# Kernel optimization log

Hardware: AMD Instinct MI355X
Metric: run time of the kernel (lower is better)

## Reference

```python
import jax, jax.numpy as jnp
import numpy as np

B, S, D, H = 4, 2048, 1024, 16
DK = D // H  # d_k = d_v = 64


def setup_inputs() -> dict:
    key = jax.random.key(0)
    ks = jax.random.split(key, 9)
    sc = 0.02
    return {
        "x": jax.random.normal(ks[0], (B, S, D), dtype=jnp.float32),
        "Wq": jax.random.normal(ks[1], (H, D, DK), dtype=jnp.float32) * sc,
        "bq": jax.random.normal(ks[2], (H, DK), dtype=jnp.float32) * sc,
        "Wk": jax.random.normal(ks[3], (H, D, DK), dtype=jnp.float32) * sc,
        "bk": jax.random.normal(ks[4], (H, DK), dtype=jnp.float32) * sc,
        "Wv": jax.random.normal(ks[5], (H, D, DK), dtype=jnp.float32) * sc,
        "bv": jax.random.normal(ks[6], (H, DK), dtype=jnp.float32) * sc,
        "Wo": jax.random.normal(ks[7], (D, D), dtype=jnp.float32) * sc,
        "bo": jax.random.normal(ks[8], (D,), dtype=jnp.float32) * sc,
    }


def reference(x, Wq, bq, Wk, bk, Wv, bv, Wo, bo):
    # per-head learned projections (heads stacked on leading axis h)
    Q = jnp.einsum("bsd,hdk->bhsk", x, Wq) + bq[None, :, None, :]
    K = jnp.einsum("bsd,hdk->bhsk", x, Wk) + bk[None, :, None, :]
    V = jnp.einsum("bsd,hdk->bhsk", x, Wv) + bv[None, :, None, :]
    scores = jnp.einsum("bhsk,bhtk->bhst", Q, K) / jnp.sqrt(jnp.float32(DK))
    # causal mask: future_sight=0, past_sight=None -> positions t > s replaced by -1e9
    s_idx = jnp.arange(S)
    causal = s_idx[:, None] >= s_idx[None, :]  # [S, S] True where allowed
    scores = jnp.where(causal[None, None, :, :], scores, jnp.float32(-1e9))
    attn = jax.nn.softmax(scores, axis=-1)
    out = jnp.einsum("bhst,bhtk->bhsk", attn, V)  # [B, H, S, DK]
    # concat heads along feature dim (head order matches ModuleList order)
    cat = out.transpose(0, 2, 1, 3).reshape(B, S, D)
    return cat @ Wo + bo
```

## Files before the change

### kernel.cpp

```cpp
#include <hip/hip_runtime.h>
#include <stdint.h>

#define B_  4
#define S_  2048
#define D_  1024
#define H_  16
#define DK_ 64
#define M_  (B_ * S_)

typedef __attribute__((ext_vector_type(8))) short bf16x8;
typedef __attribute__((ext_vector_type(4))) float f32x4;

__device__ __forceinline__ uint16_t f2bf(float f) {
    uint32_t u = __builtin_bit_cast(uint32_t, f);
    u = (u + 0x7FFFu + ((u >> 16) & 1u)) >> 16;
    return (uint16_t)u;
}

__global__ __launch_bounds__(256) void cvt_bf16_kernel(const float* __restrict__ in,
                                                       uint16_t* __restrict__ out, int n) {
    int i = (blockIdx.x * 256 + threadIdx.x) * 8;
    if (i >= n) return;
    float4 a = *(const float4*)&in[i];
    float4 b = *(const float4*)&in[i + 4];
    uint16_t o[8] = {f2bf(a.x), f2bf(a.y), f2bf(a.z), f2bf(a.w),
                     f2bf(b.x), f2bf(b.y), f2bf(b.z), f2bf(b.w)};
    *(uint4*)&out[i] = *(const uint4*)o;
}

__global__ __launch_bounds__(256) void transpose_cvt_kernel(
    const float* __restrict__ in, uint16_t* __restrict__ out, int R, int C) {
    __shared__ __align__(16) uint16_t tile[64][72];
    const int mat = blockIdx.z;
    const float* inm = in + (size_t)mat * R * C;
    uint16_t* outm = out + (size_t)mat * R * C;
    const int r0 = blockIdx.x * 64, c0 = blockIdx.y * 64;
    const int t = threadIdx.x;
    const int lr = t >> 2, lc = (t & 3) * 16;
    uint16_t tmp[16];
    #pragma unroll
    for (int j = 0; j < 16; j += 4) {
        float4 v = *(const float4*)&inm[(size_t)(r0 + lr) * C + c0 + lc + j];
        tmp[j] = f2bf(v.x); tmp[j + 1] = f2bf(v.y); tmp[j + 2] = f2bf(v.z); tmp[j + 3] = f2bf(v.w);
    }
    *(uint4*)&tile[lr][lc]     = ((const uint4*)tmp)[0];
    *(uint4*)&tile[lr][lc + 8] = ((const uint4*)tmp)[1];
    __syncthreads();
    const int oc = t >> 2, orr = (t & 3) * 16;
    uint16_t ot[16];
    #pragma unroll
    for (int j = 0; j < 16; ++j) ot[j] = tile[orr + j][oc];
    *(uint4*)&outm[(size_t)(c0 + oc) * R + r0 + orr]     = ((const uint4*)ot)[0];
    *(uint4*)&outm[(size_t)(c0 + oc) * R + r0 + orr + 8] = ((const uint4*)ot)[1];
}

__global__ __launch_bounds__(256) void qkv_mfma_kernel(
    const uint16_t* __restrict__ xb, const uint16_t* __restrict__ Wt,
    const float* __restrict__ bq, const float* __restrict__ bk, const float* __restrict__ bv,
    uint16_t* __restrict__ Q, uint16_t* __restrict__ K, uint16_t* __restrict__ V)
{
    __shared__ __align__(16) uint16_t As[128][72];
    __shared__ __align__(16) uint16_t Bs[128][72];
    const int tid = threadIdx.x;
    const int nb = blockIdx.x;
    const int sel = nb >> 3, npair = nb & 7;
    const int m0 = blockIdx.y * 128;
    const int lane = tid & 63, w = tid >> 6;
    const int wr = w >> 1, wc = w & 1;
    const int ll = lane & 15, quad = lane >> 4;

    const uint16_t* Bg = Wt + (size_t)nb * 128 * 1024;
    const float* bias = (sel == 0) ? bq : (sel == 1) ? bk : bv;
    uint16_t* Out = (sel == 0) ? Q : (sel == 1) ? K : V;

    const int ar = tid >> 1, ac = (tid & 1) * 32;

    f32x4 acc[4][4];
    const f32x4 zz = {0.f, 0.f, 0.f, 0.f};
    #pragma unroll
    for (int i = 0; i < 4; ++i)
        #pragma unroll
        for (int j = 0; j < 4; ++j) acc[i][j] = zz;

    for (int k0 = 0; k0 < 1024; k0 += 64) {
        __syncthreads();
        const uint16_t* ag = &xb[(size_t)(m0 + ar) * 1024 + k0 + ac];
        uint4 a0 = *(const uint4*)(ag);
        uint4 a1 = *(const uint4*)(ag + 8);
        uint4 a2 = *(const uint4*)(ag + 16);
        uint4 a3 = *(const uint4*)(ag + 24);
        const uint16_t* bg = &Bg[(size_t)ar * 1024 + k0 + ac];
        uint4 b0 = *(const uint4*)(bg);
        uint4 b1 = *(const uint4*)(bg + 8);
        uint4 b2 = *(const uint4*)(bg + 16);
        uint4 b3 = *(const uint4*)(bg + 24);
        *(uint4*)&As[ar][ac]      = a0;
        *(uint4*)&As[ar][ac + 8]  = a1;
        *(uint4*)&As[ar][ac + 16] = a2;
        *(uint4*)&As[ar][ac + 24] = a3;
        *(uint4*)&Bs[ar][ac]      = b0;
        *(uint4*)&Bs[ar][ac + 8]  = b1;
        *(uint4*)&Bs[ar][ac + 16] = b2;
        *(uint4*)&Bs[ar][ac + 24] = b3;
        __syncthreads();
        #pragma unroll
        for (int ks = 0; ks < 2; ++ks) {
            bf16x8 af[4], bfv[4];
            #pragma unroll
            for (int mt = 0; mt < 4; ++mt)
                af[mt] = *(const bf16x8*)&As[wr * 64 + mt * 16 + ll][ks * 32 + quad * 8];
            #pragma unroll
            for (int nt = 0; nt < 4; ++nt)
                bfv[nt] = *(const bf16x8*)&Bs[wc * 64 + nt * 16 + ll][ks * 32 + quad * 8];
            #pragma unroll
            for (int mt = 0; mt < 4; ++mt)
                #pragma unroll
                for (int nt = 0; nt < 4; ++nt)
                    acc[mt][nt] = __builtin_amdgcn_mfma_f32_16x16x32_bf16(af[mt], bfv[nt], acc[mt][nt], 0, 0, 0);
        }
    }

    const float qscale = (sel == 0) ? 0.125f : 1.0f;
    #pragma unroll
    for (int nt = 0; nt < 4; ++nt) {
        const int nl = wc * 64 + nt * 16 + ll;
        const int hh = npair * 2 + (nl >> 6);
        const int dk = nl & 63;
        const float bval = bias[npair * 128 + nl];
        #pragma unroll
        for (int mt = 0; mt < 4; ++mt) {
            #pragma unroll
            for (int r = 0; r < 4; ++r) {
                int m = m0 + wr * 64 + mt * 16 + quad * 4 + r;
                int b = m >> 11, s = m & 2047;
                float v = (acc[mt][nt][r] + bval) * qscale;
                Out[((size_t)(b * 16 + hh) * 2048 + s) * 64 + dk] = f2bf(v);
            }
        }
    }
}

__global__ __launch_bounds__(256) void attn_mfma_kernel(
    const uint16_t* __restrict__ Q, const uint16_t* __restrict__ K,
    const uint16_t* __restrict__ V, uint16_t* __restrict__ CAT)
{
    __shared__ __align__(16) uint16_t Qs[128][72];
    __shared__ __align__(16) uint16_t Ks[64][72];
    __shared__ __align__(16) uint16_t Vt[64][72];
    __shared__ __align__(16) uint16_t Ps[128][72];
    __shared__ __align__(16) float rbuf[128];

    const int tid = threadIdx.x;
    const int lane = tid & 63, w = tid >> 6;
    const int ll = lane & 15, quad = lane >> 4;
    const int bh = blockIdx.y;
    const int b = bh >> 4, h = bh & 15;

    const uint16_t* Qbh = Q + (size_t)bh * S_ * 64;
    const uint16_t* Kbh = K + (size_t)bh * S_ * 64;
    const uint16_t* Vbh = V + (size_t)bh * S_ * 64;
    uint16_t* Cbh = CAT + (size_t)b * 2048 * 1024 + h * 64;

    #pragma unroll 1
    for (int phase = 0; phase < 2; ++phase) {
        const int qtb = phase == 0 ? (15 - (int)blockIdx.x) : (int)blockIdx.x;
        const int q0 = qtb * 128;

        {
            const int r = tid >> 1, c = (tid & 1) * 32;
            const uint16_t* g = &Qbh[(size_t)(q0 + r) * 64 + c];
            uint4 v0 = *(const uint4*)g, v1 = *(const uint4*)(g + 8);
            uint4 v2 = *(const uint4*)(g + 16), v3 = *(const uint4*)(g + 24);
            *(uint4*)&Qs[r][c] = v0;      *(uint4*)&Qs[r][c + 8] = v1;
            *(uint4*)&Qs[r][c + 16] = v2; *(uint4*)&Qs[r][c + 24] = v3;
        }
        __syncthreads();

        bf16x8 qf[2][2];
        #pragma unroll
        for (int nt = 0; nt < 2; ++nt)
            #pragma unroll
            for (int ks = 0; ks < 2; ++ks)
                qf[nt][ks] = *(const bf16x8*)&Qs[w * 32 + nt * 16 + ll][ks * 32 + quad * 8];

        float l_run[2] = {0.f, 0.f};
        f32x4 oacc[2][4];
        const f32x4 zz = {0.f, 0.f, 0.f, 0.f};
        #pragma unroll
        for (int i = 0; i < 2; ++i)
            #pragma unroll
            for (int j = 0; j < 4; ++j) oacc[i][j] = zz;

        const int qw = q0 + w * 32;
        const int ktmax = 2 * qtb + 1;

        for (int kt = 0; kt <= ktmax; ++kt) {
            const int tb = kt * 64;
            __syncthreads();
            {
                const int r = tid >> 2, c = (tid & 3) * 16;
                const uint16_t* g = &Kbh[(size_t)(tb + r) * 64 + c];
                uint4 v0 = *(const uint4*)g, v1 = *(const uint4*)(g + 8);
                *(uint4*)&Ks[r][c] = v0;
                *(uint4*)&Ks[r][c + 8] = v1;
            }
            {
                const int tp = (tid & 31) * 2, d0 = (tid >> 5) * 8;
                const uint16_t* g0 = &Vbh[(size_t)(tb + tp) * 64 + d0];
                uint16_t lo[8], hi[8];
                *(uint4*)lo = *(const uint4*)g0;
                *(uint4*)hi = *(const uint4*)(g0 + 64);
                #pragma unroll
                for (int j = 0; j < 8; ++j) {
                    uint32_t pk = (uint32_t)lo[j] | ((uint32_t)hi[j] << 16);
                    *(uint32_t*)&Vt[d0 + j][tp] = pk;
                }
            }
            __syncthreads();

            const bool active = (tb <= qw + 31);
            if (active) {
                f32x4 sacc[4][2];
                #pragma unroll
                for (int i = 0; i < 4; ++i)
                    #pragma unroll
                    for (int j = 0; j < 2; ++j) sacc[i][j] = zz;
                #pragma unroll
                for (int ks = 0; ks < 2; ++ks) {
                    bf16x8 kf[4];
                    #pragma unroll
                    for (int tt = 0; tt < 4; ++tt)
                        kf[tt] = *(const bf16x8*)&Ks[tt * 16 + ll][ks * 32 + quad * 8];
                    #pragma unroll
                    for (int tt = 0; tt < 4; ++tt)
                        #pragma unroll
                        for (int nt = 0; nt < 2; ++nt)
                            sacc[tt][nt] = __builtin_amdgcn_mfma_f32_16x16x32_bf16(kf[tt], qf[nt][ks], sacc[tt][nt], 0, 0, 0);
                }
                const bool needMask = (tb + 63 > qw);
                #pragma unroll
                for (int nt = 0; nt < 2; ++nt) {
                    const int qg = qw + nt * 16 + ll;
                    float ls = 0.f;
                    #pragma unroll
                    for (int tt = 0; tt < 4; ++tt) {
                        #pragma unroll
                        for (int r = 0; r < 4; ++r) {
                            float v = sacc[tt][nt][r];
                            if (needMask) {
                                int tg = tb + tt * 16 + quad * 4 + r;
                                v = (tg > qg) ? -1e30f : v;
                            }
                            float p = __expf(v);
                            sacc[tt][nt][r] = p;
                            ls += p;
                        }
                    }
                    ls += __shfl_xor(ls, 16);
                    ls += __shfl_xor(ls, 32);
                    l_run[nt] += ls;
                    #pragma unroll
                    for (int tt = 0; tt < 4; ++tt) {
                        uint2 pv;
                        pv.x = (uint32_t)f2bf(sacc[tt][nt][0]) | ((uint32_t)f2bf(sacc[tt][nt][1]) << 16);
                        pv.y = (uint32_t)f2bf(sacc[tt][nt][2]) | ((uint32_t)f2bf(sacc[tt][nt][3]) << 16);
                        *(uint2*)&Ps[w * 32 + nt * 16 + ll][tt * 16 + quad * 4] = pv;
                    }
                }
            }
            __syncthreads();
            if (active) {
                #pragma unroll
                for (int ks = 0; ks < 2; ++ks) {
                    bf16x8 pf[2], vf[4];
                    #pragma unroll
                    for (int mt = 0; mt < 2; ++mt)
                        pf[mt] = *(const bf16x8*)&Ps[w * 32 + mt * 16 + ll][ks * 32 + quad * 8];
                    #pragma unroll
                    for (int nt = 0; nt < 4; ++nt)
                        vf[nt] = *(const bf16x8*)&Vt[nt * 16 + ll][ks * 32 + quad * 8];
                    #pragma unroll
                    for (int mt = 0; mt < 2; ++mt)
                        #pragma unroll
                        for (int nt = 0; nt < 4; ++nt)
                            oacc[mt][nt] = __builtin_amdgcn_mfma_f32_16x16x32_bf16(pf[mt], vf[nt], oacc[mt][nt], 0, 0, 0);
                }
            }
        }

        if (quad == 0) {
            rbuf[w * 32 + ll]      = 1.f / l_run[0];
            rbuf[w * 32 + 16 + ll] = 1.f / l_run[1];
        }
        __syncthreads();
        #pragma unroll
        for (int mt = 0; mt < 2; ++mt) {
            f32x4 li = *(const f32x4*)&rbuf[w * 32 + mt * 16 + quad * 4];
            #pragma unroll
            for (int r = 0; r < 4; ++r) {
                int q = q0 + w * 32 + mt * 16 + quad * 4 + r;
                #pragma unroll
                for (int nt = 0; nt < 4; ++nt) {
                    float v = oacc[mt][nt][r] * li[r];
                    Cbh[(size_t)q * 1024 + nt * 16 + ll] = f2bf(v);
                }
            }
        }
        __syncthreads();
    }
}

__global__ __launch_bounds__(256) void oproj_mfma_kernel(
    const uint16_t* __restrict__ CATb, const uint16_t* __restrict__ Wot,
    const float* __restrict__ bo, float* __restrict__ out)
{
    __shared__ __align__(16) uint16_t As[128][72];
    __shared__ __align__(16) uint16_t Bs[128][72];
    const int tid = threadIdx.x;
    const int n0 = blockIdx.x * 128;
    const int m0 = blockIdx.y * 128;
    const int lane = tid & 63, w = tid >> 6;
    const int wr = w >> 1, wc = w & 1;
    const int ll = lane & 15, quad = lane >> 4;

    const int ar = tid >> 1, ac = (tid & 1) * 32;

    f32x4 acc[4][4];
    const f32x4 zz = {0.f, 0.f, 0.f, 0.f};
    #pragma unroll
    for (int i = 0; i < 4; ++i)
        #pragma unroll
        for (int j = 0; j < 4; ++j) acc[i][j] = zz;

    for (int k0 = 0; k0 < 1024; k0 += 64) {
        __syncthreads();
        const uint16_t* ag = &CATb[(size_t)(m0 + ar) * 1024 + k0 + ac];
        uint4 a0 = *(const uint4*)(ag);
        uint4 a1 = *(const uint4*)(ag + 8);
        uint4 a2 = *(const uint4*)(ag + 16);
        uint4 a3 = *(const uint4*)(ag + 24);
        const uint16_t* bg = &Wot[(size_t)(n0 + ar) * 1024 + k0 + ac];
        uint4 b0 = *(const uint4*)(bg);
        uint4 b1 = *(const uint4*)(bg + 8);
        uint4 b2 = *(const uint4*)(bg + 16);
        uint4 b3 = *(const uint4*)(bg + 24);
        *(uint4*)&As[ar][ac]      = a0;
        *(uint4*)&As[ar][ac + 8]  = a1;
        *(uint4*)&As[ar][ac + 16] = a2;
        *(uint4*)&As[ar][ac + 24] = a3;
        *(uint4*)&Bs[ar][ac]      = b0;
        *(uint4*)&Bs[ar][ac + 8]  = b1;
        *(uint4*)&Bs[ar][ac + 16] = b2;
        *(uint4*)&Bs[ar][ac + 24] = b3;
        __syncthreads();
        #pragma unroll
        for (int ks = 0; ks < 2; ++ks) {
            bf16x8 af[4], bfv[4];
            #pragma unroll
            for (int mt = 0; mt < 4; ++mt)
                af[mt] = *(const bf16x8*)&As[wr * 64 + mt * 16 + ll][ks * 32 + quad * 8];
            #pragma unroll
            for (int nt = 0; nt < 4; ++nt)
                bfv[nt] = *(const bf16x8*)&Bs[wc * 64 + nt * 16 + ll][ks * 32 + quad * 8];
            #pragma unroll
            for (int mt = 0; mt < 4; ++mt)
                #pragma unroll
                for (int nt = 0; nt < 4; ++nt)
                    acc[mt][nt] = __builtin_amdgcn_mfma_f32_16x16x32_bf16(af[mt], bfv[nt], acc[mt][nt], 0, 0, 0);
        }
    }

    #pragma unroll
    for (int nt = 0; nt < 4; ++nt) {
        const int nl = wc * 64 + nt * 16 + ll;
        const float bval = bo[n0 + nl];
        #pragma unroll
        for (int mt = 0; mt < 4; ++mt) {
            #pragma unroll
            for (int r = 0; r < 4; ++r) {
                int m = m0 + wr * 64 + mt * 16 + quad * 4 + r;
                out[(size_t)m * 1024 + n0 + nl] = acc[mt][nt][r] + bval;
            }
        }
    }
}

extern "C" void kernel_launch(void* const* d_in, const int* in_sizes, int n_in,
                              void* d_out, int out_size, void* d_ws, size_t ws_size,
                              hipStream_t stream) {
    const float* x  = (const float*)d_in[0];
    const float* Wq = (const float*)d_in[1];
    const float* bq = (const float*)d_in[2];
    const float* Wk = (const float*)d_in[3];
    const float* bk = (const float*)d_in[4];
    const float* Wv = (const float*)d_in[5];
    const float* bv = (const float*)d_in[6];
    const float* Wo = (const float*)d_in[7];
    const float* bo = (const float*)d_in[8];

    uint8_t* p = (uint8_t*)d_ws;
    uint16_t* xb   = (uint16_t*)p; p += (size_t)M_ * D_ * 2;
    uint16_t* Wt   = (uint16_t*)p; p += (size_t)3 * H_ * DK_ * D_ * 2;
    uint16_t* Wot  = (uint16_t*)p; p += (size_t)D_ * D_ * 2;
    uint16_t* Qb   = (uint16_t*)p; p += (size_t)B_ * H_ * S_ * DK_ * 2;
    uint16_t* Kb   = (uint16_t*)p; p += (size_t)B_ * H_ * S_ * DK_ * 2;
    uint16_t* Vb   = (uint16_t*)p; p += (size_t)B_ * H_ * S_ * DK_ * 2;
    uint16_t* CATb = (uint16_t*)p;

    cvt_bf16_kernel<<<dim3((M_ * D_) / 2048), 256, 0, stream>>>(x, xb, M_ * D_);
    transpose_cvt_kernel<<<dim3(D_ / 64, 1, H_), 256, 0, stream>>>(Wq, Wt, D_, DK_);
    transpose_cvt_kernel<<<dim3(D_ / 64, 1, H_), 256, 0, stream>>>(Wk, Wt + (size_t)H_ * DK_ * D_, D_, DK_);
    transpose_cvt_kernel<<<dim3(D_ / 64, 1, H_), 256, 0, stream>>>(Wv, Wt + (size_t)2 * H_ * DK_ * D_, D_, DK_);
    transpose_cvt_kernel<<<dim3(D_ / 64, D_ / 64, 1), 256, 0, stream>>>(Wo, Wot, D_, D_);

    qkv_mfma_kernel<<<dim3(24, M_ / 128), 256, 0, stream>>>(xb, Wt, bq, bk, bv, Qb, Kb, Vb);
    attn_mfma_kernel<<<dim3(8, B_ * H_), 256, 0, stream>>>(Qb, Kb, Vb, CATb);
    oproj_mfma_kernel<<<dim3(8, M_ / 128), 256, 0, stream>>>(CATb, Wot, bo, (float*)d_out);
}
```

Before: 290.7 us.

## Store V transposed from QKV, shrink attention query tile, use exp2 softmax

The QKV projection now writes V transposed (head, dk, seq) with packed bf16 stores, so the attention kernel loads V tiles directly into LDS without the per-element transpose shuffle. The attention kernel drops to 64-query tiles per phase with Q fragments read straight from global memory, and the grid doubles to 16 blocks per head. Q is pre-scaled by log2(e)/8 so the softmax uses exp2f, and a perm-based packer replaces the scalar bf16 conversions. The new packer rounds half-up instead of to nearest-even, and the smaller tiles mean more K/V tile reloads per query in exchange for more parallelism.

```diff
diff --git a/kernel.cpp b/kernel.cpp
--- a/kernel.cpp
+++ b/kernel.cpp
@@ -11,10 +11,18 @@
 typedef __attribute__((ext_vector_type(8))) short bf16x8;
 typedef __attribute__((ext_vector_type(4))) float f32x4;
 
+#define QSCALE 0.1803368801111204f
+
 __device__ __forceinline__ uint16_t f2bf(float f) {
     uint32_t u = __builtin_bit_cast(uint32_t, f);
     u = (u + 0x7FFFu + ((u >> 16) & 1u)) >> 16;
     return (uint16_t)u;
+}
+
+__device__ __forceinline__ uint32_t pk2bf(float hi, float lo) {
+    uint32_t a = __builtin_bit_cast(uint32_t, hi) + 0x8000u;
+    uint32_t b = __builtin_bit_cast(uint32_t, lo) + 0x8000u;
+    return __builtin_amdgcn_perm(a, b, 0x07060302u);
 }
 
 __global__ __launch_bounds__(256) void cvt_bf16_kernel(const float* __restrict__ in,
@@ -71,7 +79,6 @@
 
     const uint16_t* Bg = Wt + (size_t)nb * 128 * 1024;
     const float* bias = (sel == 0) ? bq : (sel == 1) ? bk : bv;
-    uint16_t* Out = (sel == 0) ? Q : (sel == 1) ? K : V;
 
     const int ar = tid >> 1, ac = (tid & 1) * 32;
 
@@ -120,21 +127,41 @@
         }
     }
 
-    const float qscale = (sel == 0) ? 0.125f : 1.0f;
-    #pragma unroll
-    for (int nt = 0; nt < 4; ++nt) {
-        const int nl = wc * 64 + nt * 16 + ll;
-        const int hh = npair * 2 + (nl >> 6);
-        const int dk = nl & 63;
-        const float bval = bias[npair * 128 + nl];
-        #pragma unroll
-        for (int mt = 0; mt < 4; ++mt) {
-            #pragma unroll
-            for (int r = 0; r < 4; ++r) {
-                int m = m0 + wr * 64 + mt * 16 + quad * 4 + r;
+    if (sel == 2) {
+        #pragma unroll
+        for (int nt = 0; nt < 4; ++nt) {
+            const int nl = wc * 64 + nt * 16 + ll;
+            const int hh = npair * 2 + (nl >> 6);
+            const int dk = nl & 63;
+            const float bval = bias[npair * 128 + nl];
+            #pragma unroll
+            for (int mt = 0; mt < 4; ++mt) {
+                int m = m0 + wr * 64 + mt * 16 + quad * 4;
                 int b = m >> 11, s = m & 2047;
-                float v = (acc[mt][nt][r] + bval) * qscale;
-                Out[((size_t)(b * 16 + hh) * 2048 + s) * 64 + dk] = f2bf(v);
+                uint2 pv;
+                pv.x = pk2bf(acc[mt][nt][1] + bval, acc[mt][nt][0] + bval);
+                pv.y = pk2bf(acc[mt][nt][3] + bval, acc[mt][nt][2] + bval);
+                *(uint2*)&V[((size_t)(b * 16 + hh) * 64 + dk) * 2048 + s] = pv;
+            }
+        }
+    } else {
+        uint16_t* Out = (sel == 0) ? Q : K;
+        const float qs = (sel == 0) ? QSCALE : 1.0f;
+        #pragma unroll
+        for (int nt = 0; nt < 4; ++nt) {
+            const int nl = wc * 64 + nt * 16 + ll;
+            const int hh = npair * 2 + (nl >> 6);
+            const int dk = nl & 63;
+            const float bval = bias[npair * 128 + nl];
+            #pragma unroll
+            for (int mt = 0; mt < 4; ++mt) {
+                #pragma unroll
+                for (int r = 0; r < 4; ++r) {
+                    int m = m0 + wr * 64 + mt * 16 + quad * 4 + r;
+                    int b = m >> 11, s = m & 2047;
+                    float v = (acc[mt][nt][r] + bval) * qs;
+                    Out[((size_t)(b * 16 + hh) * 2048 + s) * 64 + dk] = f2bf(v);
+                }
             }
         }
     }
@@ -142,168 +169,123 @@
 
 __global__ __launch_bounds__(256) void attn_mfma_kernel(
     const uint16_t* __restrict__ Q, const uint16_t* __restrict__ K,
-    const uint16_t* __restrict__ V, uint16_t* __restrict__ CAT)
+    const uint16_t* __restrict__ Vg, uint16_t* __restrict__ CAT)
 {
-    __shared__ __align__(16) uint16_t Qs[128][72];
     __shared__ __align__(16) uint16_t Ks[64][72];
     __shared__ __align__(16) uint16_t Vt[64][72];
-    __shared__ __align__(16) uint16_t Ps[128][72];
-    __shared__ __align__(16) float rbuf[128];
+    __shared__ __align__(16) uint16_t Ps[64][72];
+    __shared__ __align__(16) float rbuf[64];
 
     const int tid = threadIdx.x;
     const int lane = tid & 63, w = tid >> 6;
     const int ll = lane & 15, quad = lane >> 4;
+    const int p = blockIdx.x;
     const int bh = blockIdx.y;
     const int b = bh >> 4, h = bh & 15;
 
     const uint16_t* Qbh = Q + (size_t)bh * S_ * 64;
     const uint16_t* Kbh = K + (size_t)bh * S_ * 64;
-    const uint16_t* Vbh = V + (size_t)bh * S_ * 64;
+    const uint16_t* Vbh = Vg + (size_t)bh * 64 * S_;
     uint16_t* Cbh = CAT + (size_t)b * 2048 * 1024 + h * 64;
+
+    const int sr = tid >> 2, sc = (tid & 3) * 16;
 
     #pragma unroll 1
     for (int phase = 0; phase < 2; ++phase) {
-        const int qtb = phase == 0 ? (15 - (int)blockIdx.x) : (int)blockIdx.x;
-        const int q0 = qtb * 128;
-
-        {
-            const int r = tid >> 1, c = (tid & 1) * 32;
-            const uint16_t* g = &Qbh[(size_t)(q0 + r) * 64 + c];
-            uint4 v0 = *(const uint4*)g, v1 = *(const uint4*)(g + 8);
-            uint4 v2 = *(const uint4*)(g + 16), v3 = *(const uint4*)(g + 24);
-            *(uint4*)&Qs[r][c] = v0;      *(uint4*)&Qs[r][c + 8] = v1;
-            *(uint4*)&Qs[r][c + 16] = v2; *(uint4*)&Qs[r][c + 24] = v3;
-        }
-        __syncthreads();
-
-        bf16x8 qf[2][2];
-        #pragma unroll
-        for (int nt = 0; nt < 2; ++nt)
-            #pragma unroll
-            for (int ks = 0; ks < 2; ++ks)
-                qf[nt][ks] = *(const bf16x8*)&Qs[w * 32 + nt * 16 + ll][ks * 32 + quad * 8];
-
-        float l_run[2] = {0.f, 0.f};
-        f32x4 oacc[2][4];
+        const int qtb = (phase == 0) ? (31 - p) : p;
+        const int q0 = qtb * 64;
+        const int qw = q0 + w * 16;
+        const int qg = qw + ll;
+
+        bf16x8 qf[2];
+        #pragma unroll
+        for (int ks = 0; ks < 2; ++ks)
+            qf[ks] = *(const bf16x8*)&Qbh[(size_t)(qw + ll) * 64 + ks * 32 + quad * 8];
+
+        float l_run = 0.f;
+        f32x4 oacc[4];
         const f32x4 zz = {0.f, 0.f, 0.f, 0.f};
         #pragma unroll
-        for (int i = 0; i < 2; ++i)
-            #pragma unroll
-            for (int j = 0; j < 4; ++j) oacc[i][j] = zz;
-
-        const int qw = q0 + w * 32;
-        const int ktmax = 2 * qtb + 1;
-
-        for (int kt = 0; kt <= ktmax; ++kt) {
+        for (int j = 0; j < 4; ++j) oacc[j] = zz;
+
+        for (int kt = 0; kt <= qtb; ++kt) {
             const int tb = kt * 64;
             __syncthreads();
             {
-                const int r = tid >> 2, c = (tid & 3) * 16;
-                const uint16_t* g = &Kbh[(size_t)(tb + r) * 64 + c];
+                const uint16_t* g = &Kbh[(size_t)(tb + sr) * 64 + sc];
                 uint4 v0 = *(const uint4*)g, v1 = *(const uint4*)(g + 8);
-                *(uint4*)&Ks[r][c] = v0;
-                *(uint4*)&Ks[r][c + 8] = v1;
+                *(uint4*)&Ks[sr][sc] = v0;
+                *(uint4*)&Ks[sr][sc + 8] = v1;
             }
             {
-                const int tp = (tid & 31) * 2, d0 = (tid >> 5) * 8;
-                const uint16_t* g0 = &Vbh[(size_t)(tb + tp) * 64 + d0];
-                uint16_t lo[8], hi[8];
-                *(uint4*)lo = *(const uint4*)g0;
-                *(uint4*)hi = *(const uint4*)(g0 + 64);
-                #pragma unroll
-                for (int j = 0; j < 8; ++j) {
-                    uint32_t pk = (uint32_t)lo[j] | ((uint32_t)hi[j] << 16);
-                    *(uint32_t*)&Vt[d0 + j][tp] = pk;
+                const uint16_t* g = &Vbh[(size_t)sr * 2048 + tb + sc];
+                uint4 v0 = *(const uint4*)g, v1 = *(const uint4*)(g + 8);
+                *(uint4*)&Vt[sr][sc] = v0;
+                *(uint4*)&Vt[sr][sc + 8] = v1;
+            }
+            __syncthreads();
+
+            f32x4 sacc[4];
+            #pragma unroll
+            for (int i = 0; i < 4; ++i) sacc[i] = zz;
+            #pragma unroll
+            for (int ks = 0; ks < 2; ++ks) {
+                #pragma unroll
+                for (int tt = 0; tt < 4; ++tt) {
+                    bf16x8 kf = *(const bf16x8*)&Ks[tt * 16 + ll][ks * 32 + quad * 8];
+                    sacc[tt] = __builtin_amdgcn_mfma_f32_16x16x32_bf16(kf, qf[ks], sacc[tt], 0, 0, 0);
                 }
             }
+
+            const bool needMask = (tb + 63 > qw);
+            float ls = 0.f;
+            #pragma unroll
+            for (int tt = 0; tt < 4; ++tt) {
+                #pragma unroll
+                for (int r = 0; r < 4; ++r) {
+                    float v = sacc[tt][r];
+                    if (needMask) {
+                        int tg = tb + tt * 16 + quad * 4 + r;
+                        v = (tg > qg) ? -1e30f : v;
+                    }
+                    float pe = exp2f(v);
+                    sacc[tt][r] = pe;
+                    ls += pe;
+                }
+            }
+            ls += __shfl_xor(ls, 16);
+            ls += __shfl_xor(ls, 32);
+            l_run += ls;
+            #pragma unroll
+            for (int tt = 0; tt < 4; ++tt) {
+                uint2 pv;
+                pv.x = pk2bf(sacc[tt][1], sacc[tt][0]);
+                pv.y = pk2bf(sacc[tt][3], sacc[tt][2]);
+                *(uint2*)&Ps[w * 16 + ll][tt * 16 + quad * 4] = pv;
+            }
             __syncthreads();
 
-            const bool active = (tb <= qw + 31);
-            if (active) {
-                f32x4 sacc[4][2];
-                #pragma unroll
-                for (int i = 0; i < 4; ++i)
-                    #pragma unroll
-                    for (int j = 0; j < 2; ++j) sacc[i][j] = zz;
-                #pragma unroll
-                for (int ks = 0; ks < 2; ++ks) {
-                    bf16x8 kf[4];
-                    #pragma unroll
-                    for (int tt = 0; tt < 4; ++tt)
-                        kf[tt] = *(const bf16x8*)&Ks[tt * 16 + ll][ks * 32 + quad * 8];
-                    #pragma unroll
-                    for (int tt = 0; tt < 4; ++tt)
-                        #pragma unroll
-                        for (int nt = 0; nt < 2; ++nt)
-                            sacc[tt][nt] = __builtin_amdgcn_mfma_f32_16x16x32_bf16(kf[tt], qf[nt][ks], sacc[tt][nt], 0, 0, 0);
+            #pragma unroll
+            for (int ks = 0; ks < 2; ++ks) {
+                bf16x8 pf = *(const bf16x8*)&Ps[w * 16 + ll][ks * 32 + quad * 8];
+                #pragma unroll
+                for (int nt = 0; nt < 4; ++nt) {
+                    bf16x8 vf = *(const bf16x8*)&Vt[nt * 16 + ll][ks * 32 + quad * 8];
+                    oacc[nt] = __builtin_amdgcn_mfma_f32_16x16x32_bf16(pf, vf, oacc[nt], 0, 0, 0);
                 }
-                const bool needMask = (tb + 63 > qw);
-                #pragma unroll
-                for (int nt = 0; nt < 2; ++nt) {
-                    const int qg = qw + nt * 16 + ll;
-                    float ls = 0.f;
-                    #pragma unroll
-                    for (int tt = 0; tt < 4; ++tt) {
-                        #pragma unroll
-                        for (int r = 0; r < 4; ++r) {
-                            float v = sacc[tt][nt][r];
-                            if (needMask) {
-                                int tg = tb + tt * 16 + quad * 4 + r;
-                                v = (tg > qg) ? -1e30f : v;
-                            }
-                            float p = __expf(v);
-                            sacc[tt][nt][r] = p;
-                            ls += p;
-                        }
-                    }
-                    ls += __shfl_xor(ls, 16);
-                    ls += __shfl_xor(ls, 32);
-                    l_run[nt] += ls;
-                    #pragma unroll
-                    for (int tt = 0; tt < 4; ++tt) {
-                        uint2 pv;
-                        pv.x = (uint32_t)f2bf(sacc[tt][nt][0]) | ((uint32_t)f2bf(sacc[tt][nt][1]) << 16);
-                        pv.y = (uint32_t)f2bf(sacc[tt][nt][2]) | ((uint32_t)f2bf(sacc[tt][nt][3]) << 16);
-                        *(uint2*)&Ps[w * 32 + nt * 16 + ll][tt * 16 + quad * 4] = pv;
-                    }
-                }
-            }
-            __syncthreads();
-            if (active) {
-                #pragma unroll
-                for (int ks = 0; ks < 2; ++ks) {
-                    bf16x8 pf[2], vf[4];
-                    #pragma unroll
-                    for (int mt = 0; mt < 2; ++mt)
-                        pf[mt] = *(const bf16x8*)&Ps[w * 32 + mt * 16 + ll][ks * 32 + quad * 8];
-                    #pragma unroll
-                    for (int nt = 0; nt < 4; ++nt)
-                        vf[nt] = *(const bf16x8*)&Vt[nt * 16 + ll][ks * 32 + quad * 8];
-                    #pragma unroll
-                    for (int mt = 0; mt < 2; ++mt)
-                        #pragma unroll
-                        for (int nt = 0; nt < 4; ++nt)
-                            oacc[mt][nt] = __builtin_amdgcn_mfma_f32_16x16x32_bf16(pf[mt], vf[nt], oacc[mt][nt], 0, 0, 0);
-                }
-            }
-        }
-
-        if (quad == 0) {
-            rbuf[w * 32 + ll]      = 1.f / l_run[0];
-            rbuf[w * 32 + 16 + ll] = 1.f / l_run[1];
-        }
-        __syncthreads();
-        #pragma unroll
-        for (int mt = 0; mt < 2; ++mt) {
-            f32x4 li = *(const f32x4*)&rbuf[w * 32 + mt * 16 + quad * 4];
-            #pragma unroll
-            for (int r = 0; r < 4; ++r) {
-                int q = q0 + w * 32 + mt * 16 + quad * 4 + r;
-                #pragma unroll
-                for (int nt = 0; nt < 4; ++nt) {
-                    float v = oacc[mt][nt][r] * li[r];
-                    Cbh[(size_t)q * 1024 + nt * 16 + ll] = f2bf(v);
-                }
+            }
+        }
+
+        if (quad == 0) rbuf[w * 16 + ll] = 1.f / l_run;
+        __syncthreads();
+        f32x4 li = *(const f32x4*)&rbuf[w * 16 + quad * 4];
+        #pragma unroll
+        for (int r = 0; r < 4; ++r) {
+            int q = q0 + w * 16 + quad * 4 + r;
+            #pragma unroll
+            for (int nt = 0; nt < 4; ++nt) {
+                float v = oacc[nt][r] * li[r];
+                Cbh[(size_t)q * 1024 + nt * 16 + ll] = f2bf(v);
             }
         }
         __syncthreads();
@@ -414,6 +396,6 @@
     transpose_cvt_kernel<<<dim3(D_ / 64, D_ / 64, 1), 256, 0, stream>>>(Wo, Wot, D_, D_);
 
     qkv_mfma_kernel<<<dim3(24, M_ / 128), 256, 0, stream>>>(xb, Wt, bq, bk, bv, Qb, Kb, Vb);
-    attn_mfma_kernel<<<dim3(8, B_ * H_), 256, 0, stream>>>(Qb, Kb, Vb, CATb);
+    attn_mfma_kernel<<<dim3(16, B_ * H_), 256, 0, stream>>>(Qb, Kb, Vb, CATb);
     oproj_mfma_kernel<<<dim3(8, M_ / 128), 256, 0, stream>>>(CATb, Wot, bo, (float*)d_out);
 }
```

Result: slower. 303.1 us (+4.2%).
